# Kernel tuning notes

Measured on AMD Instinct MI355X. Metric: run time of the kernel, lower is better.

## Reference

```python
import jax, jax.numpy as jnp
import numpy as np

SPATIAL_SHAPES = ((100, 100), (50, 50), (25, 25), (13, 13))
B, C, NH, NL, NP, DFF = 4, 256, 8, 4, 4, 1024
HD = C // NH
L = sum(h * w for h, w in SPATIAL_SHAPES)  # 13294


def _xavier(key, shape):
    s = (6.0 / (shape[0] + shape[1])) ** 0.5
    return jax.random.uniform(key, shape, jnp.float32, -s, s)


def setup_inputs():
    key = jax.random.key(0)
    ks = jax.random.split(key, 12)
    ss = jnp.array(SPATIAL_SHAPES, jnp.int32)
    lsi = jnp.concatenate([jnp.zeros((1,), jnp.int32), jnp.cumsum(ss[:, 0] * ss[:, 1])[:-1].astype(jnp.int32)])
    return {
        "query": jax.random.normal(ks[0], (B, L, C), jnp.float32),
        "query_pos": jax.random.normal(ks[1], (B, L, C), jnp.float32),
        "reference_points": jax.random.uniform(ks[2], (B, L, NL, 2), jnp.float32),
        "spatial_shapes": ss,
        "level_start_index": lsi,
        "v_W": _xavier(ks[3], (C, C)), "v_b": jnp.zeros((C,), jnp.float32),
        "off_W": 0.01 * jax.random.normal(ks[4], (C, NH * NL * NP * 2), jnp.float32),
        "off_b": 0.1 * jax.random.normal(ks[5], (NH * NL * NP * 2,), jnp.float32),
        "aw_W": 0.01 * jax.random.normal(ks[6], (C, NH * NL * NP), jnp.float32),
        "aw_b": jnp.zeros((NH * NL * NP,), jnp.float32),
        "out_W": _xavier(ks[7], (C, C)), "out_b": jnp.zeros((C,), jnp.float32),
        "ln1_g": jnp.ones((C,), jnp.float32), "ln1_b": jnp.zeros((C,), jnp.float32),
        "lin1_W": _xavier(ks[8], (C, DFF)), "lin1_b": jnp.zeros((DFF,), jnp.float32),
        "lin2_W": _xavier(ks[9], (DFF, C)), "lin2_b": jnp.zeros((C,), jnp.float32),
        "ln2_g": jnp.ones((C,), jnp.float32), "ln2_b": jnp.zeros((C,), jnp.float32),
    }


def _layer_norm(x, g, b):
    mu = x.mean(-1, keepdims=True)
    var = ((x - mu) ** 2).mean(-1, keepdims=True)
    return (x - mu) * jax.lax.rsqrt(var + 1e-5) * g + b


def _msda(q, value, reference_points, v_W, v_b, off_W, off_b, aw_W, aw_b, out_W, out_b):
    # value projection, split heads -> [B, NH, L, HD]
    v = (value @ v_W + v_b).reshape(B, L, NH, HD).transpose(0, 2, 1, 3)
    off = (q @ off_W + off_b).reshape(B, L, NH, NL, NP, 2)
    aw = jax.nn.softmax((q @ aw_W + aw_b).reshape(B, L, NH, NL * NP), axis=-1)
    aw = aw.reshape(B, L, NH, NL, NP).transpose(0, 2, 1, 3, 4)  # [B,NH,L,NL,NP]
    # offset normalizer is (W, H) per level, matching (x, y) coords
    norm = jnp.array([[w, h] for h, w in SPATIAL_SHAPES], q.dtype)
    loc = reference_points[:, :, None, :, None, :] + off / norm[None, None, None, :, None, :]
    loc = loc.transpose(0, 2, 1, 3, 4, 5)  # [B,NH,L,NL,NP,2]
    acc = jnp.zeros((B, NH, L, HD), q.dtype)
    start = 0
    for l, (H_, W_) in enumerate(SPATIAL_SHAPES):
        v_l = jax.lax.dynamic_slice_in_dim(v, start, H_ * W_, axis=2)  # [B,NH,HW,HD]
        # grid_sample(align_corners=False): pixel = loc*size - 0.5
        x = loc[:, :, :, l, :, 0] * W_ - 0.5  # [B,NH,L,NP]
        y = loc[:, :, :, l, :, 1] * H_ - 0.5
        x0 = jnp.floor(x); y0 = jnp.floor(y)
        lx = x - x0; ly = y - y0
        x0i = x0.astype(jnp.int32); y0i = y0.astype(jnp.int32)

        def corner(yi, xi, w):
            valid = (yi >= 0) & (yi < H_) & (xi >= 0) & (xi < W_)  # zero padding
            idx = jnp.clip(yi, 0, H_ - 1) * W_ + jnp.clip(xi, 0, W_ - 1)
            g = jnp.take_along_axis(v_l, idx.reshape(B, NH, L * NP, 1), axis=2)
            g = g.reshape(B, NH, L, NP, HD)
            return g * (w * valid)[..., None]

        s = (corner(y0i, x0i, (1 - ly) * (1 - lx))
             + corner(y0i, x0i + 1, (1 - ly) * lx)
             + corner(y0i + 1, x0i, ly * (1 - lx))
             + corner(y0i + 1, x0i + 1, ly * lx))  # [B,NH,L,NP,HD]
        acc = acc + (s * aw[:, :, :, l, :, None]).sum(3)
        start += H_ * W_
    out = acc.transpose(0, 2, 1, 3).reshape(B, L, C)
    return out @ out_W + out_b


def _forward(query, query_pos, reference_points, v_W, v_b, off_W, off_b, aw_W, aw_b,
             out_W, out_b, ln1_g, ln1_b, lin1_W, lin1_b, lin2_W, lin2_b, ln2_g, ln2_b):
    q = query + query_pos
    src2 = _msda(q, query, reference_points, v_W, v_b, off_W, off_b, aw_W, aw_b, out_W, out_b)
    x = _layer_norm(query + src2, ln1_g, ln1_b)
    ffn = jax.nn.relu(x @ lin1_W + lin1_b) @ lin2_W + lin2_b
    return _layer_norm(x + ffn, ln2_g, ln2_b)


def reference(query, query_pos, reference_points, spatial_shapes, level_start_index,
              v_W, v_b, off_W, off_b, aw_W, aw_b, out_W, out_b,
              ln1_g, ln1_b, lin1_W, lin1_b, lin2_W, lin2_b, ln2_g, ln2_b):
    # spatial_shapes / level_start_index are consistent with the static SPATIAL_SHAPES
    # constant (shapes must be static for reshapes under jit).
    return _forward(query, query_pos, reference_points, v_W, v_b, off_W, off_b, aw_W, aw_b,
                    out_W, out_b, ln1_g, ln1_b, lin1_W, lin1_b, lin2_W, lin2_b, ln2_g, ln2_b)
```

## Files before the change

### kernel.cpp

```cpp
#include <hip/hip_runtime.h>
#include <hip/hip_bf16.h>
#include <cstddef>

constexpr int Ll   = 13294;
constexpr int NROW = 4 * Ll;
constexpr int MP   = 53248;

typedef __bf16       bf8v __attribute__((ext_vector_type(8)));
typedef float        f4v  __attribute__((ext_vector_type(4)));
typedef unsigned int u4v  __attribute__((ext_vector_type(4)));

template<bool RELU, bool OUTF, bool OUTB>
__global__ __launch_bounds__(256)
void gemm_mfma(const __hip_bfloat16* __restrict__ A, const __hip_bfloat16* __restrict__ Bt,
               const float* __restrict__ bias, const float* __restrict__ bias2,
               float* __restrict__ Cf, __hip_bfloat16* __restrict__ Cb,
               int M, int N, int K)
{
    __shared__ __hip_bfloat16 As[128 * 32];
    __shared__ __hip_bfloat16 Bs[128 * 32];
    const int tid  = threadIdx.x;
    const int wid  = tid >> 6;
    const int lane = tid & 63;
    const int m0 = blockIdx.y * 128;
    const int n0 = blockIdx.x * 128;
    const int wm = wid >> 1, wn = wid & 1;
    const int fr = lane & 15, fq = lane >> 4;
    const int sr = lane >> 2;
    const int sc = (lane & 3) * 8;

    f4v acc[4][4] = {};

    for (int k0 = 0; k0 < K; k0 += 32) {
        #pragma unroll
        for (int i = 0; i < 2; ++i) {
            const int s = wid * 2 + i;
            const __hip_bfloat16* sa = A  + (size_t)(m0 + s * 16 + sr) * K + k0 + sc;
            const __hip_bfloat16* sb = Bt + (size_t)(n0 + s * 16 + sr) * K + k0 + sc;
            __builtin_amdgcn_global_load_lds(
                (const __attribute__((address_space(1))) void*)sa,
                (__attribute__((address_space(3))) void*)&As[s * 512], 16, 0, 0);
            __builtin_amdgcn_global_load_lds(
                (const __attribute__((address_space(1))) void*)sb,
                (__attribute__((address_space(3))) void*)&Bs[s * 512], 16, 0, 0);
        }
        __syncthreads();

        bf8v a[4], b[4];
        #pragma unroll
        for (int r = 0; r < 4; ++r) {
            a[r] = __builtin_bit_cast(bf8v, *(const u4v*)&As[(wm * 64 + r * 16 + fr) * 32 + fq * 8]);
            b[r] = __builtin_bit_cast(bf8v, *(const u4v*)&Bs[(wn * 64 + r * 16 + fr) * 32 + fq * 8]);
        }
        #pragma unroll
        for (int nr = 0; nr < 4; ++nr)
            #pragma unroll
            for (int mr = 0; mr < 4; ++mr)
                acc[nr][mr] = __builtin_amdgcn_mfma_f32_16x16x32_bf16(b[nr], a[mr], acc[nr][mr], 0, 0, 0);
        __syncthreads();
    }

    #pragma unroll
    for (int nr = 0; nr < 4; ++nr) {
        const int colbase = n0 + wn * 64 + nr * 16 + fq * 4;
        const float* bp = (bias2 != nullptr && colbase >= 256) ? (bias2 - 256) : bias;
        const float4 b4 = *(const float4*)&bp[colbase];
        #pragma unroll
        for (int mr = 0; mr < 4; ++mr) {
            const int row = m0 + wm * 64 + mr * 16 + fr;
            f4v v = acc[nr][mr];
            v[0] += b4.x; v[1] += b4.y; v[2] += b4.z; v[3] += b4.w;
            if (RELU) {
                v[0] = fmaxf(v[0], 0.f); v[1] = fmaxf(v[1], 0.f);
                v[2] = fmaxf(v[2], 0.f); v[3] = fmaxf(v[3], 0.f);
            }
            if (OUTF)
                *(float4*)&Cf[(size_t)row * N + colbase] = make_float4(v[0], v[1], v[2], v[3]);
            if (OUTB) {
                union { ushort4 u; __hip_bfloat16 h[4]; } pk;
                pk.h[0] = __float2bfloat16(v[0]); pk.h[1] = __float2bfloat16(v[1]);
                pk.h[2] = __float2bfloat16(v[2]); pk.h[3] = __float2bfloat16(v[3]);
                *(ushort4*)&Cb[(size_t)row * N + colbase] = pk.u;
            }
        }
    }
}

template<bool STOREB, bool RESB>
__global__ __launch_bounds__(256)
void gemm_ln(const __hip_bfloat16* __restrict__ A, const __hip_bfloat16* __restrict__ Bt,
             const float* __restrict__ bias,
             const float* __restrict__ resF, const __hip_bfloat16* __restrict__ resB,
             int Mres,
             const float* __restrict__ g, const float* __restrict__ be,
             float* __restrict__ outF, int MstoreF,
             __hip_bfloat16* __restrict__ outB,
             int K)
{
    __shared__ __hip_bfloat16 As[64 * 32];
    __shared__ __hip_bfloat16 Bs[256 * 32];
    __shared__ float red[2][64][2];
    const int tid  = threadIdx.x;
    const int wid  = tid >> 6;
    const int lane = tid & 63;
    const int m0 = blockIdx.x * 64;
    const int wm = wid >> 1, wn = wid & 1;
    const int fr = lane & 15, fq = lane >> 4;
    const int sr = lane >> 2;
    const int sc = (lane & 3) * 8;

    f4v acc[8][2] = {};

    for (int k0 = 0; k0 < K; k0 += 32) {
        {
            const __hip_bfloat16* sa = A + (size_t)(m0 + wid * 16 + sr) * K + k0 + sc;
            __builtin_amdgcn_global_load_lds(
                (const __attribute__((address_space(1))) void*)sa,
                (__attribute__((address_space(3))) void*)&As[wid * 512], 16, 0, 0);
        }
        #pragma unroll
        for (int i = 0; i < 4; ++i) {
            const int s = wid * 4 + i;
            const __hip_bfloat16* sb = Bt + (size_t)(s * 16 + sr) * K + k0 + sc;
            __builtin_amdgcn_global_load_lds(
                (const __attribute__((address_space(1))) void*)sb,
                (__attribute__((address_space(3))) void*)&Bs[s * 512], 16, 0, 0);
        }
        __syncthreads();

        bf8v a[2], b[8];
        #pragma unroll
        for (int r = 0; r < 2; ++r)
            a[r] = __builtin_bit_cast(bf8v, *(const u4v*)&As[(wm * 32 + r * 16 + fr) * 32 + fq * 8]);
        #pragma unroll
        for (int r = 0; r < 8; ++r)
            b[r] = __builtin_bit_cast(bf8v, *(const u4v*)&Bs[(wn * 128 + r * 16 + fr) * 32 + fq * 8]);
        #pragma unroll
        for (int nr = 0; nr < 8; ++nr)
            #pragma unroll
            for (int mr = 0; mr < 2; ++mr)
                acc[nr][mr] = __builtin_amdgcn_mfma_f32_16x16x32_bf16(b[nr], a[mr], acc[nr][mr], 0, 0, 0);
        __syncthreads();
    }

    float s2[2] = {}, q2[2] = {};
    #pragma unroll
    for (int nr = 0; nr < 8; ++nr) {
        const int colbase = wn * 128 + nr * 16 + fq * 4;
        const float4 b4 = *(const float4*)&bias[colbase];
        #pragma unroll
        for (int mr = 0; mr < 2; ++mr) {
            const int row = m0 + wm * 32 + mr * 16 + fr;
            f4v x = acc[nr][mr];
            x[0] += b4.x; x[1] += b4.y; x[2] += b4.z; x[3] += b4.w;
            if (RESB) {
                const ushort4 r4 = *(const ushort4*)&resB[(size_t)row * 256 + colbase];
                x[0] += __builtin_bit_cast(float, (unsigned)r4.x << 16);
                x[1] += __builtin_bit_cast(float, (unsigned)r4.y << 16);
                x[2] += __builtin_bit_cast(float, (unsigned)r4.z << 16);
                x[3] += __builtin_bit_cast(float, (unsigned)r4.w << 16);
            } else if (row < Mres) {
                const float4 r4 = *(const float4*)&resF[(size_t)row * 256 + colbase];
                x[0] += r4.x; x[1] += r4.y; x[2] += r4.z; x[3] += r4.w;
            }
            acc[nr][mr] = x;
            s2[mr] += x[0] + x[1] + x[2] + x[3];
            q2[mr] += x[0]*x[0] + x[1]*x[1] + x[2]*x[2] + x[3]*x[3];
        }
    }
    #pragma unroll
    for (int mr = 0; mr < 2; ++mr) {
        s2[mr] += __shfl_xor(s2[mr], 16, 64);
        q2[mr] += __shfl_xor(q2[mr], 16, 64);
        s2[mr] += __shfl_xor(s2[mr], 32, 64);
        q2[mr] += __shfl_xor(q2[mr], 32, 64);
    }
    if (fq == 0) {
        #pragma unroll
        for (int mr = 0; mr < 2; ++mr) {
            red[wn][wm * 32 + mr * 16 + fr][0] = s2[mr];
            red[wn][wm * 32 + mr * 16 + fr][1] = q2[mr];
        }
    }
    __syncthreads();
    float mean[2], rinv[2];
    #pragma unroll
    for (int mr = 0; mr < 2; ++mr) {
        const int r = wm * 32 + mr * 16 + fr;
        const float ss = red[0][r][0] + red[1][r][0];
        const float qq = red[0][r][1] + red[1][r][1];
        mean[mr] = ss * (1.f / 256.f);
        const float var = qq * (1.f / 256.f) - mean[mr] * mean[mr];
        rinv[mr] = rsqrtf(var + 1e-5f);
    }
    #pragma unroll
    for (int nr = 0; nr < 8; ++nr) {
        const int colbase = wn * 128 + nr * 16 + fq * 4;
        const float4 g4 = *(const float4*)&g[colbase];
        const float4 e4 = *(const float4*)&be[colbase];
        #pragma unroll
        for (int mr = 0; mr < 2; ++mr) {
            const int row = m0 + wm * 32 + mr * 16 + fr;
            const f4v x = acc[nr][mr];
            float y0 = (x[0] - mean[mr]) * rinv[mr] * g4.x + e4.x;
            float y1 = (x[1] - mean[mr]) * rinv[mr] * g4.y + e4.y;
            float y2 = (x[2] - mean[mr]) * rinv[mr] * g4.z + e4.z;
            float y3 = (x[3] - mean[mr]) * rinv[mr] * g4.w + e4.w;
            if (row < MstoreF)
                *(float4*)&outF[(size_t)row * 256 + colbase] = make_float4(y0, y1, y2, y3);
            if (STOREB) {
                union { ushort4 u; __hip_bfloat16 h[4]; } pk;
                pk.h[0] = __float2bfloat16(y0); pk.h[1] = __float2bfloat16(y1);
                pk.h[2] = __float2bfloat16(y2); pk.h[3] = __float2bfloat16(y3);
                *(ushort4*)&outB[(size_t)row * 256 + colbase] = pk.u;
            }
        }
    }
}

__global__ __launch_bounds__(256)
void prep_weights(const float* __restrict__ vW, const float* __restrict__ offW,
                  const float* __restrict__ awW, const float* __restrict__ outW,
                  const float* __restrict__ w1, const float* __restrict__ w2,
                  __hip_bfloat16* __restrict__ vWt, __hip_bfloat16* __restrict__ catWt,
                  __hip_bfloat16* __restrict__ outWt, __hip_bfloat16* __restrict__ w1t,
                  __hip_bfloat16* __restrict__ w2t)
{
    int i = blockIdx.x * 256 + threadIdx.x;
    if (i < 65536) { const int n = i >> 8, k = i & 255;
        vWt[i] = __float2bfloat16(vW[(size_t)k * 256 + n]); return; }
    i -= 65536;
    if (i < 98304) { const int n = i >> 8, k = i & 255;
        catWt[i] = __float2bfloat16(n < 256 ? offW[(size_t)k * 256 + n]
                                            : awW[(size_t)k * 128 + n - 256]); return; }
    i -= 98304;
    if (i < 65536) { const int n = i >> 8, k = i & 255;
        outWt[i] = __float2bfloat16(outW[(size_t)k * 256 + n]); return; }
    i -= 65536;
    if (i < 262144) { const int n = i >> 8, k = i & 255;
        w1t[i] = __float2bfloat16(w1[(size_t)k * 1024 + n]); return; }
    i -= 262144;
    { const int n = i >> 10, k = i & 1023;
        w2t[i] = __float2bfloat16(w2[(size_t)k * 256 + n]); }
}

__global__ __launch_bounds__(256)
void cvt_both(const float* __restrict__ q, const float* __restrict__ qp,
              __hip_bfloat16* __restrict__ qb, __hip_bfloat16* __restrict__ qpb)
{
    const int i   = blockIdx.x * 256 + threadIdx.x;
    const int row = i >> 5;
    union { u4v u; __hip_bfloat16 h[8]; } p1, p2;
    if (row >= NROW) {
        u4v z = {0u, 0u, 0u, 0u};
        p1.u = z; p2.u = z;
    } else {
        const size_t e = (size_t)i * 8;
        float4 x0 = *(const float4*)&q[e];
        float4 x1 = *(const float4*)&q[e + 4];
        float4 y0 = *(const float4*)&qp[e];
        float4 y1 = *(const float4*)&qp[e + 4];
        p1.h[0] = __float2bfloat16(x0.x); p1.h[1] = __float2bfloat16(x0.y);
        p1.h[2] = __float2bfloat16(x0.z); p1.h[3] = __float2bfloat16(x0.w);
        p1.h[4] = __float2bfloat16(x1.x); p1.h[5] = __float2bfloat16(x1.y);
        p1.h[6] = __float2bfloat16(x1.z); p1.h[7] = __float2bfloat16(x1.w);
        p2.h[0] = __float2bfloat16(x0.x + y0.x); p2.h[1] = __float2bfloat16(x0.y + y0.y);
        p2.h[2] = __float2bfloat16(x0.z + y0.z); p2.h[3] = __float2bfloat16(x0.w + y0.w);
        p2.h[4] = __float2bfloat16(x1.x + y1.x); p2.h[5] = __float2bfloat16(x1.y + y1.y);
        p2.h[6] = __float2bfloat16(x1.z + y1.z); p2.h[7] = __float2bfloat16(x1.w + y1.w);
    }
    *(u4v*)&qb[(size_t)i * 8]  = p1.u;
    *(u4v*)&qpb[(size_t)i * 8] = p2.u;
}

__device__ __forceinline__ float blo(unsigned u) { return __builtin_bit_cast(float, u << 16); }
__device__ __forceinline__ float bhi(unsigned u) { return __builtin_bit_cast(float, u & 0xffff0000u); }

__global__ __launch_bounds__(256)
void msda_sample3(const __hip_bfloat16* __restrict__ v, const float* __restrict__ cat,
                  const float* __restrict__ refp, __hip_bfloat16* __restrict__ accO)
{
    __shared__ int   sIdx[1024][4];
    __shared__ float sW[1024][4];
    const int row0 = blockIdx.x * 8;
    const int tid  = threadIdx.x;

    #pragma unroll
    for (int it = 0; it < 4; ++it) {
        const int item = it * 256 + tid;
        const int p = item & 15, h = (item >> 4) & 7, r = item >> 7;
        const int row = row0 + r;
        const int lvl = p >> 2;
        const float logit = cat[(size_t)row * 384 + 256 + h * 16 + p];
        float mx = logit;
        #pragma unroll
        for (int o = 1; o < 16; o <<= 1) mx = fmaxf(mx, __shfl_xor(mx, o, 64));
        const float e = __expf(logit - mx);
        float s = e;
        #pragma unroll
        for (int o = 1; o < 16; o <<= 1) s += __shfl_xor(s, o, 64);
        const float aw = e / s;

        const int Hs[4] = {100, 50, 25, 13};
        const int Ss[4] = {0, 10000, 12500, 13125};
        const int   Wl = Hs[lvl];
        const float Wf = (float)Wl;
        const float ox = cat[(size_t)row * 384 + h * 32 + p * 2 + 0];
        const float oy = cat[(size_t)row * 384 + h * 32 + p * 2 + 1];
        const float rx = refp[(size_t)row * 8 + lvl * 2 + 0];
        const float ry = refp[(size_t)row * 8 + lvl * 2 + 1];
        const float x = (rx + ox / Wf) * Wf - 0.5f;
        const float y = (ry + oy / Wf) * Wf - 0.5f;
        const float x0f = floorf(x), y0f = floorf(y);
        const float lx = x - x0f, ly = y - y0f;
        const int x0 = (int)x0f, y0 = (int)y0f;
        const int b = row / Ll;
        const int vbase = b * Ll + Ss[lvl];
        int ixr[4]; float wr[4];
        #pragma unroll
        for (int c = 0; c < 4; ++c) {
            const int cy = c >> 1, cx = c & 1;
            const int yi = y0 + cy, xi = x0 + cx;
            const bool ok = (yi >= 0) & (yi < Wl) & (xi >= 0) & (xi < Wl);
            const int yc = min(max(yi, 0), Wl - 1);
            const int xc = min(max(xi, 0), Wl - 1);
            const float wt = (cy ? ly : 1.f - ly) * (cx ? lx : 1.f - lx);
            ixr[c] = (vbase + yc * Wl + xc) * 512;
            wr[c]  = ok ? aw * wt : 0.f;
        }
        const int item2 = (item & ~15) | ((item & 15) ^ h);
        *(int4*)&sIdx[item2][0] = make_int4(ixr[0], ixr[1], ixr[2], ixr[3]);
        *(float4*)&sW[item2][0] = make_float4(wr[0], wr[1], wr[2], wr[3]);
    }
    __syncthreads();

    const int r   = tid >> 5;
    const int h   = (tid >> 2) & 7;
    const int oct = tid & 3;
    const int row = row0 + r;
    const char* vB = (const char*)v + (h * 32 + oct * 8) * 2;
    const int ibase = r * 128 + h * 16;
    float acc[8] = {};
    #pragma unroll
    for (int i = 0; i < 16; ++i) {
        const int idx = ibase + (i ^ h);
        const int4   ix = *(const int4*)&sIdx[idx][0];
        const float4 wv = *(const float4*)&sW[idx][0];
        u4v u0 = *(const u4v*)(vB + (unsigned)ix.x);
        u4v u1 = *(const u4v*)(vB + (unsigned)ix.y);
        u4v u2 = *(const u4v*)(vB + (unsigned)ix.z);
        u4v u3 = *(const u4v*)(vB + (unsigned)ix.w);
        #pragma unroll
        for (int q = 0; q < 4; ++q) {
            acc[2*q]   = fmaf(wv.x, blo(u0[q]), acc[2*q]);
            acc[2*q+1] = fmaf(wv.x, bhi(u0[q]), acc[2*q+1]);
            acc[2*q]   = fmaf(wv.y, blo(u1[q]), acc[2*q]);
            acc[2*q+1] = fmaf(wv.y, bhi(u1[q]), acc[2*q+1]);
            acc[2*q]   = fmaf(wv.z, blo(u2[q]), acc[2*q]);
            acc[2*q+1] = fmaf(wv.z, bhi(u2[q]), acc[2*q+1]);
            acc[2*q]   = fmaf(wv.w, blo(u3[q]), acc[2*q]);
            acc[2*q+1] = fmaf(wv.w, bhi(u3[q]), acc[2*q+1]);
        }
    }
    union { u4v u; __hip_bfloat16 hh[8]; } pk;
    #pragma unroll
    for (int q = 0; q < 8; ++q) pk.hh[q] = __float2bfloat16(acc[q]);
    *(u4v*)&accO[(size_t)row * 256 + h * 32 + oct * 8] = pk.u;
}

extern "C" void kernel_launch(void* const* d_in, const int* in_sizes, int n_in,
                              void* d_out, int out_size, void* d_ws, size_t ws_size,
                              hipStream_t stream)
{
    (void)in_sizes; (void)n_in; (void)out_size; (void)ws_size;
    const float* query = (const float*)d_in[0];
    const float* qpos  = (const float*)d_in[1];
    const float* refp  = (const float*)d_in[2];
    const float* v_W   = (const float*)d_in[5];
    const float* v_b   = (const float*)d_in[6];
    const float* off_W = (const float*)d_in[7];
    const float* off_b = (const float*)d_in[8];
    const float* aw_W  = (const float*)d_in[9];
    const float* aw_b  = (const float*)d_in[10];
    const float* out_W = (const float*)d_in[11];
    const float* out_b = (const float*)d_in[12];
    const float* ln1g  = (const float*)d_in[13];
    const float* ln1b  = (const float*)d_in[14];
    const float* w1    = (const float*)d_in[15];
    const float* b1    = (const float*)d_in[16];
    const float* w2    = (const float*)d_in[17];
    const float* b2    = (const float*)d_in[18];
    const float* ln2g  = (const float*)d_in[19];
    const float* ln2b  = (const float*)d_in[20];
    float* out = (float*)d_out;

    char* ws = (char*)d_ws;
    constexpr size_t CATF_B = (size_t)MP * 384 * 4;
    constexpr size_t HALF_B = (size_t)MP * 256 * 2;
    float*          catf = (float*)ws;
    __hip_bfloat16* qb   = (__hip_bfloat16*)(ws + CATF_B);
    __hip_bfloat16* qpb  = (__hip_bfloat16*)(ws + CATF_B + HALF_B);
    __hip_bfloat16* vbuf = (__hip_bfloat16*)(ws + CATF_B + 2 * HALF_B);
    __hip_bfloat16* accb = qb;
    __hip_bfloat16* xb   = vbuf;
    __hip_bfloat16* hbuf = (__hip_bfloat16*)ws;
    char* wsw = ws + CATF_B + 3 * HALF_B;
    __hip_bfloat16* vWt   = (__hip_bfloat16*)(wsw);
    __hip_bfloat16* catWt = (__hip_bfloat16*)(wsw + 131072);
    __hip_bfloat16* outWt = (__hip_bfloat16*)(wsw + 327680);
    __hip_bfloat16* w1t   = (__hip_bfloat16*)(wsw + 458752);
    __hip_bfloat16* w2t   = (__hip_bfloat16*)(wsw + 983040);

    dim3 blk(256);

    prep_weights<<<2944, blk, 0, stream>>>(v_W, off_W, aw_W, out_W, w1, w2,
                                           vWt, catWt, outWt, w1t, w2t);
    cvt_both<<<MP / 8, blk, 0, stream>>>(query, qpos, qb, qpb);

    gemm_mfma<false, false, true><<<dim3(2, MP / 128), blk, 0, stream>>>(
        qb, vWt, v_b, nullptr, nullptr, vbuf, MP, 256, 256);
    gemm_mfma<false, true, false><<<dim3(3, MP / 128), blk, 0, stream>>>(
        qpb, catWt, off_b, aw_b, catf, nullptr, MP, 384, 256);

    msda_sample3<<<NROW / 8, blk, 0, stream>>>(vbuf, catf, refp, accb);

    gemm_ln<true, false><<<MP / 64, blk, 0, stream>>>(
        accb, outWt, out_b, query, nullptr, NROW, ln1g, ln1b,
        nullptr, 0, xb, 256);

    gemm_mfma<true, false, true><<<dim3(8, MP / 128), blk, 0, stream>>>(
        xb, w1t, b1, nullptr, nullptr, hbuf, MP, 1024, 256);

    gemm_ln<false, true><<<MP / 64, blk, 0, stream>>>(
        hbuf, w2t, b2, nullptr, xb, MP, ln2g, ln2b,
        out, NROW, nullptr, 1024);
}
```

Measured before the change: 364.2 us.

## Fuse FFN into one kernel and fold fp32-to-bf16 input conversion into projection GEMMs

The FFN's two GEMMs become one kernel. It computes relu(x·W1) in 128-column chunks into an XOR-swizzled LDS tile and accumulates the second GEMM plus residual and LayerNorm directly, so the 1024-wide hidden activation is never written to or read from global memory. The separate cvt_both kernel is removed: the value and offset/attention projection GEMMs now load fp32 query (and query_pos) themselves, add them and convert to bf16 when filling LDS. This saves a kernel launch and an intermediate buffer round trip, at the cost of synchronous register-staged A loads instead of async global_load_lds. The fused FFN re-reads the xb tile for each of its 8 chunks and runs only 832 blocks, which may limit overlap.

```diff
diff --git a/kernel.cpp b/kernel.cpp
--- a/kernel.cpp
+++ b/kernel.cpp
@@ -10,12 +10,12 @@
 typedef float        f4v  __attribute__((ext_vector_type(4)));
 typedef unsigned int u4v  __attribute__((ext_vector_type(4)));
 
-template<bool RELU, bool OUTF, bool OUTB>
+template<bool ADD2, bool OUTF, bool OUTB>
 __global__ __launch_bounds__(256)
-void gemm_mfma(const __hip_bfloat16* __restrict__ A, const __hip_bfloat16* __restrict__ Bt,
+void gemm_proj(const float* __restrict__ Af, const float* __restrict__ Af2,
+               const __hip_bfloat16* __restrict__ Bt,
                const float* __restrict__ bias, const float* __restrict__ bias2,
-               float* __restrict__ Cf, __hip_bfloat16* __restrict__ Cb,
-               int M, int N, int K)
+               float* __restrict__ Cf, __hip_bfloat16* __restrict__ Cb, int N)
 {
     __shared__ __hip_bfloat16 As[128 * 32];
     __shared__ __hip_bfloat16 Bs[128 * 32];
@@ -31,15 +31,42 @@
 
     f4v acc[4][4] = {};
 
-    for (int k0 = 0; k0 < K; k0 += 32) {
+    for (int k0 = 0; k0 < 256; k0 += 32) {
+        {
+            const int row = tid >> 1;
+            const int h2  = (tid & 1) << 4;
+            const int gr  = m0 + row;
+            union { u4v u[2]; __hip_bfloat16 h[16]; } pk;
+            if (gr < NROW) {
+                const float* src = Af + (size_t)gr * 256 + k0 + h2;
+                float x[16];
+                *(float4*)&x[0]  = ((const float4*)src)[0];
+                *(float4*)&x[4]  = ((const float4*)src)[1];
+                *(float4*)&x[8]  = ((const float4*)src)[2];
+                *(float4*)&x[12] = ((const float4*)src)[3];
+                if (ADD2) {
+                    const float* s2 = Af2 + (size_t)gr * 256 + k0 + h2;
+                    float y[16];
+                    *(float4*)&y[0]  = ((const float4*)s2)[0];
+                    *(float4*)&y[4]  = ((const float4*)s2)[1];
+                    *(float4*)&y[8]  = ((const float4*)s2)[2];
+                    *(float4*)&y[12] = ((const float4*)s2)[3];
+                    #pragma unroll
+                    for (int j = 0; j < 16; ++j) x[j] += y[j];
+                }
+                #pragma unroll
+                for (int j = 0; j < 16; ++j) pk.h[j] = __float2bfloat16(x[j]);
+            } else {
+                u4v z = {0u, 0u, 0u, 0u};
+                pk.u[0] = z; pk.u[1] = z;
+            }
+            *(u4v*)&As[row * 32 + h2]     = pk.u[0];
+            *(u4v*)&As[row * 32 + h2 + 8] = pk.u[1];
+        }
         #pragma unroll
         for (int i = 0; i < 2; ++i) {
             const int s = wid * 2 + i;
-            const __hip_bfloat16* sa = A  + (size_t)(m0 + s * 16 + sr) * K + k0 + sc;
-            const __hip_bfloat16* sb = Bt + (size_t)(n0 + s * 16 + sr) * K + k0 + sc;
-            __builtin_amdgcn_global_load_lds(
-                (const __attribute__((address_space(1))) void*)sa,
-                (__attribute__((address_space(3))) void*)&As[s * 512], 16, 0, 0);
+            const __hip_bfloat16* sb = Bt + (size_t)(n0 + s * 16 + sr) * 256 + k0 + sc;
             __builtin_amdgcn_global_load_lds(
                 (const __attribute__((address_space(1))) void*)sb,
                 (__attribute__((address_space(3))) void*)&Bs[s * 512], 16, 0, 0);
@@ -70,10 +97,6 @@
             const int row = m0 + wm * 64 + mr * 16 + fr;
             f4v v = acc[nr][mr];
             v[0] += b4.x; v[1] += b4.y; v[2] += b4.z; v[3] += b4.w;
-            if (RELU) {
-                v[0] = fmaxf(v[0], 0.f); v[1] = fmaxf(v[1], 0.f);
-                v[2] = fmaxf(v[2], 0.f); v[3] = fmaxf(v[3], 0.f);
-            }
             if (OUTF)
                 *(float4*)&Cf[(size_t)row * N + colbase] = make_float4(v[0], v[1], v[2], v[3]);
             if (OUTB) {
@@ -86,16 +109,11 @@
     }
 }
 
-template<bool STOREB, bool RESB>
 __global__ __launch_bounds__(256)
-void gemm_ln(const __hip_bfloat16* __restrict__ A, const __hip_bfloat16* __restrict__ Bt,
-             const float* __restrict__ bias,
-             const float* __restrict__ resF, const __hip_bfloat16* __restrict__ resB,
-             int Mres,
-             const float* __restrict__ g, const float* __restrict__ be,
-             float* __restrict__ outF, int MstoreF,
-             __hip_bfloat16* __restrict__ outB,
-             int K)
+void gemm_ln_out(const __hip_bfloat16* __restrict__ A, const __hip_bfloat16* __restrict__ Bt,
+                 const float* __restrict__ bias, const float* __restrict__ resF,
+                 const float* __restrict__ g, const float* __restrict__ be,
+                 __hip_bfloat16* __restrict__ outB)
 {
     __shared__ __hip_bfloat16 As[64 * 32];
     __shared__ __hip_bfloat16 Bs[256 * 32];
@@ -111,9 +129,9 @@
 
     f4v acc[8][2] = {};
 
-    for (int k0 = 0; k0 < K; k0 += 32) {
+    for (int k0 = 0; k0 < 256; k0 += 32) {
         {
-            const __hip_bfloat16* sa = A + (size_t)(m0 + wid * 16 + sr) * K + k0 + sc;
+            const __hip_bfloat16* sa = A + (size_t)(m0 + wid * 16 + sr) * 256 + k0 + sc;
             __builtin_amdgcn_global_load_lds(
                 (const __attribute__((address_space(1))) void*)sa,
                 (__attribute__((address_space(3))) void*)&As[wid * 512], 16, 0, 0);
@@ -121,7 +139,7 @@
         #pragma unroll
         for (int i = 0; i < 4; ++i) {
             const int s = wid * 4 + i;
-            const __hip_bfloat16* sb = Bt + (size_t)(s * 16 + sr) * K + k0 + sc;
+            const __hip_bfloat16* sb = Bt + (size_t)(s * 16 + sr) * 256 + k0 + sc;
             __builtin_amdgcn_global_load_lds(
                 (const __attribute__((address_space(1))) void*)sb,
                 (__attribute__((address_space(3))) void*)&Bs[s * 512], 16, 0, 0);
@@ -153,13 +171,7 @@
             const int row = m0 + wm * 32 + mr * 16 + fr;
             f4v x = acc[nr][mr];
             x[0] += b4.x; x[1] += b4.y; x[2] += b4.z; x[3] += b4.w;
-            if (RESB) {
-                const ushort4 r4 = *(const ushort4*)&resB[(size_t)row * 256 + colbase];
-                x[0] += __builtin_bit_cast(float, (unsigned)r4.x << 16);
-                x[1] += __builtin_bit_cast(float, (unsigned)r4.y << 16);
-                x[2] += __builtin_bit_cast(float, (unsigned)r4.z << 16);
-                x[3] += __builtin_bit_cast(float, (unsigned)r4.w << 16);
-            } else if (row < Mres) {
+            if (row < NROW) {
                 const float4 r4 = *(const float4*)&resF[(size_t)row * 256 + colbase];
                 x[0] += r4.x; x[1] += r4.y; x[2] += r4.z; x[3] += r4.w;
             }
@@ -202,18 +214,177 @@
         for (int mr = 0; mr < 2; ++mr) {
             const int row = m0 + wm * 32 + mr * 16 + fr;
             const f4v x = acc[nr][mr];
+            union { ushort4 u; __hip_bfloat16 h[4]; } pk;
+            pk.h[0] = __float2bfloat16((x[0] - mean[mr]) * rinv[mr] * g4.x + e4.x);
+            pk.h[1] = __float2bfloat16((x[1] - mean[mr]) * rinv[mr] * g4.y + e4.y);
+            pk.h[2] = __float2bfloat16((x[2] - mean[mr]) * rinv[mr] * g4.z + e4.z);
+            pk.h[3] = __float2bfloat16((x[3] - mean[mr]) * rinv[mr] * g4.w + e4.w);
+            *(ushort4*)&outB[(size_t)row * 256 + colbase] = pk.u;
+        }
+    }
+}
+
+__global__ __launch_bounds__(256)
+void ffn_fused(const __hip_bfloat16* __restrict__ xb,
+               const __hip_bfloat16* __restrict__ w1t,
+               const __hip_bfloat16* __restrict__ w2t,
+               const float* __restrict__ b1, const float* __restrict__ b2,
+               const float* __restrict__ g, const float* __restrict__ be,
+               float* __restrict__ out)
+{
+    __shared__ __hip_bfloat16 As[64 * 32];
+    __shared__ __hip_bfloat16 Bs1[128 * 32];
+    __shared__ __hip_bfloat16 Hs[64 * 128];
+    __shared__ __hip_bfloat16 Bs2[256 * 32];
+    __shared__ float red[2][64][2];
+    const int tid  = threadIdx.x;
+    const int wid  = tid >> 6;
+    const int lane = tid & 63;
+    const int m0 = blockIdx.x * 64;
+    const int wm = wid >> 1, wn = wid & 1;
+    const int fr = lane & 15, fq = lane >> 4;
+    const int sr = lane >> 2;
+    const int sc = (lane & 3) * 8;
+
+    f4v acc_o[8][2] = {};
+
+    for (int c = 0; c < 8; ++c) {
+        f4v acc_h[4][2] = {};
+        for (int k0 = 0; k0 < 256; k0 += 32) {
+            {
+                const __hip_bfloat16* sa = xb + (size_t)(m0 + wid * 16 + sr) * 256 + k0 + sc;
+                __builtin_amdgcn_global_load_lds(
+                    (const __attribute__((address_space(1))) void*)sa,
+                    (__attribute__((address_space(3))) void*)&As[wid * 512], 16, 0, 0);
+            }
+            #pragma unroll
+            for (int i = 0; i < 2; ++i) {
+                const int s = wid * 2 + i;
+                const __hip_bfloat16* sb = w1t + (size_t)(c * 128 + s * 16 + sr) * 256 + k0 + sc;
+                __builtin_amdgcn_global_load_lds(
+                    (const __attribute__((address_space(1))) void*)sb,
+                    (__attribute__((address_space(3))) void*)&Bs1[s * 512], 16, 0, 0);
+            }
+            __syncthreads();
+            bf8v a[2], b[4];
+            #pragma unroll
+            for (int r = 0; r < 2; ++r)
+                a[r] = __builtin_bit_cast(bf8v, *(const u4v*)&As[(wm * 32 + r * 16 + fr) * 32 + fq * 8]);
+            #pragma unroll
+            for (int r = 0; r < 4; ++r)
+                b[r] = __builtin_bit_cast(bf8v, *(const u4v*)&Bs1[(wn * 64 + r * 16 + fr) * 32 + fq * 8]);
+            #pragma unroll
+            for (int nr = 0; nr < 4; ++nr)
+                #pragma unroll
+                for (int mr = 0; mr < 2; ++mr)
+                    acc_h[nr][mr] = __builtin_amdgcn_mfma_f32_16x16x32_bf16(b[nr], a[mr], acc_h[nr][mr], 0, 0, 0);
+            __syncthreads();
+        }
+        #pragma unroll
+        for (int nr = 0; nr < 4; ++nr) {
+            const int colb = wn * 64 + nr * 16 + fq * 4;
+            const float4 b4 = *(const float4*)&b1[c * 128 + colb];
+            #pragma unroll
+            for (int mr = 0; mr < 2; ++mr) {
+                const int row = wm * 32 + mr * 16 + fr;
+                const f4v h = acc_h[nr][mr];
+                union { ushort4 u; __hip_bfloat16 hh[4]; } pk;
+                pk.hh[0] = __float2bfloat16(fmaxf(h[0] + b4.x, 0.f));
+                pk.hh[1] = __float2bfloat16(fmaxf(h[1] + b4.y, 0.f));
+                pk.hh[2] = __float2bfloat16(fmaxf(h[2] + b4.z, 0.f));
+                pk.hh[3] = __float2bfloat16(fmaxf(h[3] + b4.w, 0.f));
+                const int col8 = (colb >> 3) ^ (row & 7);
+                *(ushort4*)((char*)Hs + row * 256 + col8 * 16 + (colb & 7) * 2) = pk.u;
+            }
+        }
+        for (int k1 = 0; k1 < 128; k1 += 32) {
+            #pragma unroll
+            for (int i = 0; i < 4; ++i) {
+                const int s = wid * 4 + i;
+                const __hip_bfloat16* sb = w2t + (size_t)(s * 16 + sr) * 1024 + c * 128 + k1 + sc;
+                __builtin_amdgcn_global_load_lds(
+                    (const __attribute__((address_space(1))) void*)sb,
+                    (__attribute__((address_space(3))) void*)&Bs2[s * 512], 16, 0, 0);
+            }
+            __syncthreads();
+            bf8v ah[2], b[8];
+            #pragma unroll
+            for (int r = 0; r < 2; ++r) {
+                const int row = wm * 32 + r * 16 + fr;
+                const int col8 = ((k1 >> 3) + fq) ^ (row & 7);
+                ah[r] = __builtin_bit_cast(bf8v, *(const u4v*)((const char*)Hs + row * 256 + col8 * 16));
+            }
+            #pragma unroll
+            for (int r = 0; r < 8; ++r)
+                b[r] = __builtin_bit_cast(bf8v, *(const u4v*)&Bs2[(wn * 128 + r * 16 + fr) * 32 + fq * 8]);
+            #pragma unroll
+            for (int nr = 0; nr < 8; ++nr)
+                #pragma unroll
+                for (int mr = 0; mr < 2; ++mr)
+                    acc_o[nr][mr] = __builtin_amdgcn_mfma_f32_16x16x32_bf16(b[nr], ah[mr], acc_o[nr][mr], 0, 0, 0);
+            __syncthreads();
+        }
+    }
+
+    float s2[2] = {}, q2[2] = {};
+    #pragma unroll
+    for (int nr = 0; nr < 8; ++nr) {
+        const int colbase = wn * 128 + nr * 16 + fq * 4;
+        const float4 b4 = *(const float4*)&b2[colbase];
+        #pragma unroll
+        for (int mr = 0; mr < 2; ++mr) {
+            const int row = m0 + wm * 32 + mr * 16 + fr;
+            f4v x = acc_o[nr][mr];
+            const ushort4 r4 = *(const ushort4*)&xb[(size_t)row * 256 + colbase];
+            x[0] += b4.x + __builtin_bit_cast(float, (unsigned)r4.x << 16);
+            x[1] += b4.y + __builtin_bit_cast(float, (unsigned)r4.y << 16);
+            x[2] += b4.z + __builtin_bit_cast(float, (unsigned)r4.z << 16);
+            x[3] += b4.w + __builtin_bit_cast(float, (unsigned)r4.w << 16);
+            acc_o[nr][mr] = x;
+            s2[mr] += x[0] + x[1] + x[2] + x[3];
+            q2[mr] += x[0]*x[0] + x[1]*x[1] + x[2]*x[2] + x[3]*x[3];
+        }
+    }
+    #pragma unroll
+    for (int mr = 0; mr < 2; ++mr) {
+        s2[mr] += __shfl_xor(s2[mr], 16, 64);
+        q2[mr] += __shfl_xor(q2[mr], 16, 64);
+        s2[mr] += __shfl_xor(s2[mr], 32, 64);
+        q2[mr] += __shfl_xor(q2[mr], 32, 64);
+    }
+    if (fq == 0) {
+        #pragma unroll
+        for (int mr = 0; mr < 2; ++mr) {
+            red[wn][wm * 32 + mr * 16 + fr][0] = s2[mr];
+            red[wn][wm * 32 + mr * 16 + fr][1] = q2[mr];
+        }
+    }
+    __syncthreads();
+    float mean[2], rinv[2];
+    #pragma unroll
+    for (int mr = 0; mr < 2; ++mr) {
+        const int r = wm * 32 + mr * 16 + fr;
+        const float ss = red[0][r][0] + red[1][r][0];
+        const float qq = red[0][r][1] + red[1][r][1];
+        mean[mr] = ss * (1.f / 256.f);
+        const float var = qq * (1.f / 256.f) - mean[mr] * mean[mr];
+        rinv[mr] = rsqrtf(var + 1e-5f);
+    }
+    #pragma unroll
+    for (int nr = 0; nr < 8; ++nr) {
+        const int colbase = wn * 128 + nr * 16 + fq * 4;
+        const float4 g4 = *(const float4*)&g[colbase];
+        const float4 e4 = *(const float4*)&be[colbase];
+        #pragma unroll
+        for (int mr = 0; mr < 2; ++mr) {
+            const int row = m0 + wm * 32 + mr * 16 + fr;
+            if (row >= NROW) continue;
+            const f4v x = acc_o[nr][mr];
             float y0 = (x[0] - mean[mr]) * rinv[mr] * g4.x + e4.x;
             float y1 = (x[1] - mean[mr]) * rinv[mr] * g4.y + e4.y;
             float y2 = (x[2] - mean[mr]) * rinv[mr] * g4.z + e4.z;
             float y3 = (x[3] - mean[mr]) * rinv[mr] * g4.w + e4.w;
-            if (row < MstoreF)
-                *(float4*)&outF[(size_t)row * 256 + colbase] = make_float4(y0, y1, y2, y3);
-            if (STOREB) {
-                union { ushort4 u; __hip_bfloat16 h[4]; } pk;
-                pk.h[0] = __float2bfloat16(y0); pk.h[1] = __float2bfloat16(y1);
-                pk.h[2] = __float2bfloat16(y2); pk.h[3] = __float2bfloat16(y3);
-                *(ushort4*)&outB[(size_t)row * 256 + colbase] = pk.u;
-            }
+            *(float4*)&out[(size_t)row * 256 + colbase] = make_float4(y0, y1, y2, y3);
         }
     }
 }
@@ -244,35 +415,6 @@
         w2t[i] = __float2bfloat16(w2[(size_t)k * 256 + n]); }
 }
 
-__global__ __launch_bounds__(256)
-void cvt_both(const float* __restrict__ q, const float* __restrict__ qp,
-              __hip_bfloat16* __restrict__ qb, __hip_bfloat16* __restrict__ qpb)
-{
-    const int i   = blockIdx.x * 256 + threadIdx.x;
-    const int row = i >> 5;
-    union { u4v u; __hip_bfloat16 h[8]; } p1, p2;
-    if (row >= NROW) {
-        u4v z = {0u, 0u, 0u, 0u};
-        p1.u = z; p2.u = z;
-    } else {
-        const size_t e = (size_t)i * 8;
-        float4 x0 = *(const float4*)&q[e];
-        float4 x1 = *(const float4*)&q[e + 4];
-        float4 y0 = *(const float4*)&qp[e];
-        float4 y1 = *(const float4*)&qp[e + 4];
-        p1.h[0] = __float2bfloat16(x0.x); p1.h[1] = __float2bfloat16(x0.y);
-        p1.h[2] = __float2bfloat16(x0.z); p1.h[3] = __float2bfloat16(x0.w);
-        p1.h[4] = __float2bfloat16(x1.x); p1.h[5] = __float2bfloat16(x1.y);
-        p1.h[6] = __float2bfloat16(x1.z); p1.h[7] = __float2bfloat16(x1.w);
-        p2.h[0] = __float2bfloat16(x0.x + y0.x); p2.h[1] = __float2bfloat16(x0.y + y0.y);
-        p2.h[2] = __float2bfloat16(x0.z + y0.z); p2.h[3] = __float2bfloat16(x0.w + y0.w);
-        p2.h[4] = __float2bfloat16(x1.x + y1.x); p2.h[5] = __float2bfloat16(x1.y + y1.y);
-        p2.h[6] = __float2bfloat16(x1.z + y1.z); p2.h[7] = __float2bfloat16(x1.w + y1.w);
-    }
-    *(u4v*)&qb[(size_t)i * 8]  = p1.u;
-    *(u4v*)&qpb[(size_t)i * 8] = p2.u;
-}
-
 __device__ __forceinline__ float blo(unsigned u) { return __builtin_bit_cast(float, u << 16); }
 __device__ __forceinline__ float bhi(unsigned u) { return __builtin_bit_cast(float, u & 0xffff0000u); }
 
@@ -301,9 +443,9 @@
         for (int o = 1; o < 16; o <<= 1) s += __shfl_xor(s, o, 64);
         const float aw = e / s;
 
-        const int Hs[4] = {100, 50, 25, 13};
-        const int Ss[4] = {0, 10000, 12500, 13125};
-        const int   Wl = Hs[lvl];
+        const int Hs_[4] = {100, 50, 25, 13};
+        const int Ss[4]  = {0, 10000, 12500, 13125};
+        const int   Wl = Hs_[lvl];
         const float Wf = (float)Wl;
         const float ox = cat[(size_t)row * 384 + h * 32 + p * 2 + 0];
         const float oy = cat[(size_t)row * 384 + h * 32 + p * 2 + 1];
@@ -398,13 +540,10 @@
     constexpr size_t CATF_B = (size_t)MP * 384 * 4;
     constexpr size_t HALF_B = (size_t)MP * 256 * 2;
     float*          catf = (float*)ws;
-    __hip_bfloat16* qb   = (__hip_bfloat16*)(ws + CATF_B);
-    __hip_bfloat16* qpb  = (__hip_bfloat16*)(ws + CATF_B + HALF_B);
-    __hip_bfloat16* vbuf = (__hip_bfloat16*)(ws + CATF_B + 2 * HALF_B);
-    __hip_bfloat16* accb = qb;
+    __hip_bfloat16* accb = (__hip_bfloat16*)(ws + CATF_B);
+    __hip_bfloat16* vbuf = (__hip_bfloat16*)(ws + CATF_B + HALF_B);
     __hip_bfloat16* xb   = vbuf;
-    __hip_bfloat16* hbuf = (__hip_bfloat16*)ws;
-    char* wsw = ws + CATF_B + 3 * HALF_B;
+    char* wsw = ws + CATF_B + 2 * HALF_B;
     __hip_bfloat16* vWt   = (__hip_bfloat16*)(wsw);
     __hip_bfloat16* catWt = (__hip_bfloat16*)(wsw + 131072);
     __hip_bfloat16* outWt = (__hip_bfloat16*)(wsw + 327680);
@@ -415,23 +554,17 @@
 
     prep_weights<<<2944, blk, 0, stream>>>(v_W, off_W, aw_W, out_W, w1, w2,
                                            vWt, catWt, outWt, w1t, w2t);
-    cvt_both<<<MP / 8, blk, 0, stream>>>(query, qpos, qb, qpb);
-
-    gemm_mfma<false, false, true><<<dim3(2, MP / 128), blk, 0, stream>>>(
-        qb, vWt, v_b, nullptr, nullptr, vbuf, MP, 256, 256);
-    gemm_mfma<false, true, false><<<dim3(3, MP / 128), blk, 0, stream>>>(
-        qpb, catWt, off_b, aw_b, catf, nullptr, MP, 384, 256);
+
+    gemm_proj<false, false, true><<<dim3(2, MP / 128), blk, 0, stream>>>(
+        query, nullptr, vWt, v_b, nullptr, nullptr, vbuf, 256);
+    gemm_proj<true, true, false><<<dim3(3, MP / 128), blk, 0, stream>>>(
+        query, qpos, catWt, off_b, aw_b, catf, nullptr, 384);
 
     msda_sample3<<<NROW / 8, blk, 0, stream>>>(vbuf, catf, refp, accb);
 
-    gemm_ln<true, false><<<MP / 64, blk, 0, stream>>>(
-        accb, outWt, out_b, query, nullptr, NROW, ln1g, ln1b,
-        nullptr, 0, xb, 256);
-
-    gemm_mfma<true, false, true><<<dim3(8, MP / 128), blk, 0, stream>>>(
-        xb, w1t, b1, nullptr, nullptr, hbuf, MP, 1024, 256);
-
-    gemm_ln<false, true><<<MP / 64, blk, 0, stream>>>(
-        hbuf, w2t, b2, nullptr, xb, MP, ln2g, ln2b,
-        out, NROW, nullptr, 1024);
+    gemm_ln_out<<<MP / 64, blk, 0, stream>>>(
+        accb, outWt, out_b, query, ln1g, ln1b, xb);
+
+    ffn_fused<<<MP / 64, blk, 0, stream>>>(
+        xb, w1t, w2t, b1, b2, ln2g, ln2b, out);
 }
```

Measured after the change: 449.0 us. +23.3%, slower.
